# Kernel optimization log

Hardware: AMD Instinct MI355X
Metric: run time of the kernel (lower is better)

Reference implementation:

```python
import jax, jax.numpy as jnp
import numpy as np
from jax import lax

B, IMG, CIN, C, HEADS, K = 2, 112, 64, 256, 8, 3  # kernel_size[0]=3 used by hatt1
HD = C // HEADS


def layer_norm(x, w, b, eps=1e-5):
    mu = jnp.mean(x, axis=-1, keepdims=True)
    var = jnp.mean((x - mu) ** 2, axis=-1, keepdims=True)
    return (x - mu) / jnp.sqrt(var + eps) * w + b


def conv3x3(x, w, b):
    # x: (B,Cin,H,W), w: (Cout,Cin,3,3) -- stride 1, pad 1 (OverlapPatchEmbed patchsize=3)
    y = lax.conv_general_dilated(x, w, (1, 1), ((1, 1), (1, 1)),
                                 dimension_numbers=('NCHW', 'OIHW', 'NCHW'))
    return y + b[None, :, None, None]


def nat_cross_attention(q_in, kv_in, wq, bq, wkv, bkv, rpb, wp, bp, heads=HEADS, k=K):
    # NATTEN-style 2D neighborhood attention with separate query / key-value maps.
    Bb, H, W, Cc = q_in.shape
    hd = Cc // heads
    scale = hd ** -0.5
    q = (q_in @ wq + bq).reshape(Bb, H, W, heads, hd) * scale
    kv = (kv_in @ wkv + bkv).reshape(Bb, H, W, 2, heads, hd)
    kk, v = kv[:, :, :, 0], kv[:, :, :, 1]
    half = k // 2
    # border-clamped window starts -> every pixel attends to a full k x k window
    si = jnp.clip(jnp.arange(H) - half, 0, H - k)  # (H,)
    sj = jnp.clip(jnp.arange(W) - half, 0, W - k)  # (W,)
    nbi = si[:, None] + jnp.arange(k)  # (H,k) neighbor rows
    nbj = sj[:, None] + jnp.arange(k)  # (W,k) neighbor cols

    def gather(t):  # t: (B,H,W,heads,hd) -> (B,H,W,heads,k*k,hd)
        g = t[:, nbi]            # (B,H,k,W,heads,hd)
        g = g[:, :, :, nbj]      # (B,H,k,W,k,heads,hd)
        return jnp.transpose(g, (0, 1, 3, 5, 2, 4, 6)).reshape(Bb, H, W, heads, k * k, hd)

    kg, vg = gather(kk), gather(v)
    logits = jnp.einsum('bijhd,bijhnd->bijhn', q, kg)
    # relative position bias: rpb (heads, 2k-1, 2k-1)
    pi = jnp.arange(H) - si  # query position inside its window, 0..k-1
    pj = jnp.arange(W) - sj
    idx_i = jnp.arange(k)[None, :] - pi[:, None] + (k - 1)  # (H,k) in [0, 2k-2]
    idx_j = jnp.arange(k)[None, :] - pj[:, None] + (k - 1)  # (W,k)
    bias = rpb[:, idx_i]           # (heads,H,k,2k-1)
    bias = bias[:, :, :, idx_j]    # (heads,H,k,W,k)
    bias = jnp.transpose(bias, (1, 3, 0, 2, 4)).reshape(H, W, heads, k * k)
    attn = jax.nn.softmax(logits + bias, axis=-1)
    out = jnp.einsum('bijhn,bijhnd->bijhd', attn, vg).reshape(Bb, H, W, Cc)
    return out @ wp + bp


def setup_inputs() -> dict:
    key = jax.random.key(0)
    ks = jax.random.split(key, 24)
    std = 0.02
    inp = {
        'xq': jax.random.normal(ks[0], (B, CIN, IMG, IMG), jnp.float32),
        'xkv': jax.random.normal(ks[1], (B, CIN, IMG, IMG), jnp.float32),
        'conv1_w': jax.random.normal(ks[2], (C, CIN, 3, 3), jnp.float32) * std,
        'conv1_b': jnp.zeros((C,), jnp.float32),
        'conv3_w': jax.random.normal(ks[3], (C, CIN, 3, 3), jnp.float32) * std,
        'conv3_b': jnp.zeros((C,), jnp.float32),
        'ln1_w': jnp.ones((C,), jnp.float32), 'ln1_b': jnp.zeros((C,), jnp.float32),
        'ln10_w': jnp.ones((C,), jnp.float32), 'ln10_b': jnp.zeros((C,), jnp.float32),
        'ln3_w': jnp.ones((C,), jnp.float32), 'ln3_b': jnp.zeros((C,), jnp.float32),
        'wq': jax.random.normal(ks[4], (C, C), jnp.float32) * std,
        'bq': jnp.zeros((C,), jnp.float32),
        'wkv': jax.random.normal(ks[5], (C, 2 * C), jnp.float32) * std,
        'bkv': jnp.zeros((2 * C,), jnp.float32),
        'rpb': jax.random.normal(ks[6], (HEADS, 2 * K - 1, 2 * K - 1), jnp.float32) * std,
        'wp': jax.random.normal(ks[7], (C, C), jnp.float32) * std,
        'bp': jnp.zeros((C,), jnp.float32),
        'fc1_w': jax.random.normal(ks[8], (C, 2 * C), jnp.float32) * std,
        'fc1_b': jnp.zeros((2 * C,), jnp.float32),
        'fc2_w': jax.random.normal(ks[9], (2 * C, C), jnp.float32) * std,
        'fc2_b': jnp.zeros((C,), jnp.float32),
    }
    return inp


def reference(xq, xkv, conv1_w, conv1_b, conv3_w, conv3_b, ln1_w, ln1_b, ln10_w, ln10_b,
              ln3_w, ln3_b, wq, bq, wkv, bkv, rpb, wp, bp, fc1_w, fc1_b, fc2_w, fc2_b):
    # patch embeds (stride-1 3x3 conv, pad 1), channels-last maps (B,H,W,C)
    x1 = jnp.transpose(conv3x3(xq, conv1_w, conv1_b), (0, 2, 3, 1))
    x3 = jnp.transpose(conv3x3(xkv, conv3_w, conv3_b), (0, 2, 3, 1))
    qn = layer_norm(x1, ln1_w, ln1_b)    # norm1(x_embedding1)
    kvn = layer_norm(x1, ln10_w, ln10_b)  # norm1_0(x_embedding1)
    att1 = nat_cross_attention(qn, kvn, wq, bq, wkv, bkv, rpb, wp, bp)
    att = att1 + x3  # drop_path is identity at inference
    h = layer_norm(att, ln3_w, ln3_b)
    m = jax.nn.gelu(h @ fc1_w + fc1_b, approximate=False) @ fc2_w + fc2_b
    x = m + att
    return jnp.transpose(x, (0, 3, 1, 2))  # (B,C,H,W)
```

## Files before the change

kernel.cpp:

```cpp
#include <hip/hip_runtime.h>
#include <math.h>

#define IMG 112
#define CIN 64
#define CH 256
#define PADW 114
#define IMG2 12544
#define NPIX 25088
#define SCQ 0.17677669529663687f

typedef __bf16 bf16;
typedef __bf16 bf16x8 __attribute__((ext_vector_type(8)));
typedef float f32x4 __attribute__((ext_vector_type(4)));

__device__ __forceinline__ void gld_lds16(const void* g, void* l) {
    __builtin_amdgcn_global_load_lds(
        (const __attribute__((address_space(1))) void*)g,
        (__attribute__((address_space(3))) void*)l,
        16, 0, 0);
}
#define VMCNT0() asm volatile("s_waitcnt vmcnt(0)" ::: "memory")
#define BAR() __builtin_amdgcn_s_barrier()

__global__ __launch_bounds__(256) void prep_kernel(
    const float* __restrict__ xq, const float* __restrict__ xkv,
    bf16* __restrict__ padq, bf16* __restrict__ padkv,
    const float* __restrict__ c1w, const float* __restrict__ c3w,
    bf16* __restrict__ cw1, bf16* __restrict__ cw2,
    const float* __restrict__ wq, bf16* __restrict__ wqt,
    const float* __restrict__ wkv, bf16* __restrict__ wkvt,
    const float* __restrict__ wp, bf16* __restrict__ wpt,
    const float* __restrict__ f1w, bf16* __restrict__ wf1,
    const float* __restrict__ f2w, bf16* __restrict__ wf2) {
    int bid = blockIdx.x, tid = threadIdx.x;
    __shared__ float lds[CIN * 113];
    if (bid < 448) {
        const float* in = (bid < 224) ? xq : xkv;
        bf16* out = (bid < 224) ? padq : padkv;
        int bi = (bid < 224) ? bid : bid - 224;
        int b = bi / IMG, i = bi % IMG;
        const float* src = in + (size_t)b * CIN * IMG2 + (size_t)i * IMG;
        for (int t = tid; t < CIN * IMG; t += 256) {
            int ci = t / IMG, j = t - ci * IMG;
            lds[ci * 113 + j] = src[(size_t)ci * IMG2 + j];
        }
        __syncthreads();
        bf16* dst = out + (((size_t)(b * PADW + (i + 1)) * PADW) + 1) * CIN;
        for (int t = tid; t < CIN * IMG; t += 256) {
            int j = t / CIN, ci = t - j * CIN;
            dst[(size_t)j * CIN + ci] = (bf16)lds[ci * 113 + j];
        }
        bf16* rowbase = out + ((size_t)(b * PADW + (i + 1)) * PADW) * CIN;
        if (tid < 128) rowbase[(tid >> 6 ? 113 * CIN : 0) + (tid & 63)] = (bf16)0.0f;
        if (i == 0)
            for (int t = tid; t < PADW * CIN; t += 256)
                out[((size_t)(b * PADW + 0) * PADW) * CIN + t] = (bf16)0.0f;
        if (i == IMG - 1)
            for (int t = tid; t < PADW * CIN; t += 256)
                out[((size_t)(b * PADW + 113) * PADW) * CIN + t] = (bf16)0.0f;
    } else if (bid < 1024) {
        int idx = (bid - 448) * 256 + tid;
        int co = idx / 576, r = idx - co * 576;
        int tap = r >> 6, ci = r & 63;
        int src = co * 576 + ci * 9 + tap;
        cw1[idx] = (bf16)c1w[src];
        cw2[idx] = (bf16)c3w[src];
    } else {
        int off = (bid - 1024) * 256 + tid;
        const float* in; bf16* out; int K, N; float sc = 1.0f; int base;
        if (off < 65536)       { in = wq;  out = wqt;  K = 256; N = 256; sc = SCQ; base = 0; }
        else if (off < 196608) { in = wkv; out = wkvt; K = 256; N = 512; base = 65536; }
        else if (off < 262144) { in = wp;  out = wpt;  K = 256; N = 256; base = 196608; }
        else if (off < 393216) { in = f1w; out = wf1;  K = 256; N = 512; base = 262144; }
        else                   { in = f2w; out = wf2;  K = 512; N = 256; base = 393216; }
        int idx = off - base;
        int n = idx / K, k = idx - n * K;
        out[idx] = (bf16)(in[(size_t)k * N + n] * sc);
    }
}

#define M_DENSE 0
#define M_LN2   1
#define M_WPLN  2
#define M_GELU  3
#define M_NCHW  4

template <int AMODE, int MODE>
__device__ __forceinline__ void gemm_core(
    char* sm,
    const bf16* __restrict__ A, const bf16* __restrict__ B,
    const float* __restrict__ bias, float bscale,
    const bf16* __restrict__ res,
    bf16* __restrict__ out0, int ldo0,
    bf16* __restrict__ out1, float* __restrict__ outf,
    const float* __restrict__ lnw0, const float* __restrict__ lnb0,
    const float* __restrict__ lnw1, const float* __restrict__ lnb1,
    int K) {
    bf16* As = (bf16*)sm;
    bf16* Bs = (bf16*)(sm + 16384);
    float* lnb = (float*)sm;
    float* T = (float*)(sm + 2048);

    const int tid = threadIdx.x;
    const int wave = tid >> 6, lane = tid & 63;
    const int m0 = blockIdx.x * 64;
    const int wm = wave >> 1, wn = wave & 1;
    const int fr = lane & 15, fq = lane >> 4;
    const int srow = lane >> 3;
    const int scol = ((lane & 7) ^ srow) * 8;

    const bf16* aptr[2];
#pragma unroll
    for (int q = 0; q < 2; ++q) {
        int arow = m0 + wave * 16 + q * 8 + srow;
        if (AMODE == 1) {
            int b = arow / IMG2;
            int rem = arow - b * IMG2;
            int i = rem / IMG, j = rem - i * IMG;
            aptr[q] = A + ((size_t)((b * PADW + i) * PADW + j)) * CIN + scol;
        } else {
            aptr[q] = A + (size_t)arow * K + scol;
        }
    }
    const bf16* bptr0 = B + (size_t)(wave * 64 + srow) * K + scol;

    auto STAGE = [&](int bi, int kt) {
        int aoff = (AMODE == 1) ? ((kt / 3) * PADW + (kt - (kt / 3) * 3)) * CIN : kt * 64;
        int boff = kt * 64;
        bf16* ad = As + bi * 4096 + (wave * 16) * 64;
        gld_lds16(aptr[0] + aoff, ad);
        gld_lds16(aptr[1] + aoff, ad + 8 * 64);
        bf16* bd = Bs + bi * 16384 + (wave * 64) * 64;
#pragma unroll
        for (int u = 0; u < 8; ++u)
            gld_lds16(bptr0 + (size_t)u * 8 * K + boff, bd + u * 8 * 64);
    };

    f32x4 acc[2][8] = {};
    auto COMPUTE = [&](int bi) {
        const bf16* ab = As + bi * 4096;
        const bf16* bb = Bs + bi * 16384;
#pragma unroll
        for (int ks = 0; ks < 2; ++ks) {
            int ch = ((ks * 4 + fq) ^ (fr & 7)) * 8;
            bf16x8 af[2];
#pragma unroll
            for (int mi = 0; mi < 2; ++mi) af[mi] = *(const bf16x8*)&ab[(wm * 32 + mi * 16 + fr) * 64 + ch];
            bf16x8 bv[8];
#pragma unroll
            for (int ni = 0; ni < 8; ++ni) bv[ni] = *(const bf16x8*)&bb[(wn * 128 + ni * 16 + fr) * 64 + ch];
#pragma unroll
            for (int mi = 0; mi < 2; ++mi)
#pragma unroll
                for (int ni = 0; ni < 8; ++ni)
                    acc[mi][ni] = __builtin_amdgcn_mfma_f32_16x16x32_bf16(af[mi], bv[ni], acc[mi][ni], 0, 0, 0);
        }
    };

    const int nk = K >> 6;
    STAGE(0, 0);
    VMCNT0();
    BAR();
    int cur = 0;
    for (int kt = 0; kt < nk - 1; ++kt) {
        STAGE(cur ^ 1, kt + 1);
        COMPUTE(cur);
        VMCNT0();
        BAR();
        cur ^= 1;
    }
    COMPUTE(cur);

    float bvv[8];
#pragma unroll
    for (int ni = 0; ni < 8; ++ni) bvv[ni] = bias[wn * 128 + ni * 16 + fr] * bscale;
#pragma unroll
    for (int mi = 0; mi < 2; ++mi)
#pragma unroll
        for (int ni = 0; ni < 8; ++ni)
#pragma unroll
            for (int r = 0; r < 4; ++r) {
                float x = acc[mi][ni][r] + bvv[ni];
                if (MODE == M_WPLN) {
                    int prow = m0 + wm * 32 + mi * 16 + fq * 4 + r;
                    int col = wn * 128 + ni * 16 + fr;
                    x += (float)res[(size_t)prow * 256 + col];
                }
                if (MODE == M_GELU) x = 0.5f * x * (1.0f + erff(x * 0.70710678118f));
                acc[mi][ni][r] = x;
            }

    float mean_[2][4], rstd_[2][4];
    if (MODE == M_LN2 || MODE == M_WPLN) {
        BAR();
#pragma unroll
        for (int mi = 0; mi < 2; ++mi)
#pragma unroll
            for (int r = 0; r < 4; ++r) {
                float s = 0.0f, ss = 0.0f;
#pragma unroll
                for (int ni = 0; ni < 8; ++ni) {
                    float x = acc[mi][ni][r];
                    s += x; ss += x * x;
                }
#pragma unroll
                for (int msk = 1; msk <= 8; msk <<= 1) {
                    s += __shfl_xor(s, msk);
                    ss += __shfl_xor(ss, msk);
                }
                if (fr == 0) {
                    int row = wm * 32 + mi * 16 + fq * 4 + r;
                    lnb[wn * 128 + row] = s;
                    lnb[wn * 128 + 64 + row] = ss;
                }
            }
        BAR();
#pragma unroll
        for (int mi = 0; mi < 2; ++mi)
#pragma unroll
            for (int r = 0; r < 4; ++r) {
                int row = wm * 32 + mi * 16 + fq * 4 + r;
                float s = lnb[row] + lnb[128 + row];
                float ss = lnb[64 + row] + lnb[192 + row];
                float mean = s * (1.0f / CH);
                float var = ss * (1.0f / CH) - mean * mean;
                mean_[mi][r] = mean;
                rstd_[mi][r] = rsqrtf(var + 1e-5f);
            }
    } else {
        BAR();
    }

#pragma unroll
    for (int mi = 0; mi < 2; ++mi)
#pragma unroll
        for (int ni = 0; ni < 8; ++ni)
#pragma unroll
            for (int r = 0; r < 4; ++r) {
                int row = wm * 32 + mi * 16 + fq * 4 + r;
                int col = wn * 128 + ni * 16 + fr;
                float x = acc[mi][ni][r];
                if (MODE == M_LN2) x = (x - mean_[mi][r]) * rstd_[mi][r];
                T[row * 257 + col] = x;
            }
    BAR();

    if (MODE == M_NCHW) {
        int c = tid;
        int b = m0 / IMG2, p0 = m0 - b * IMG2;
        float* outp = outf + ((size_t)(b * CH + c)) * IMG2 + p0;
        const bf16* rp = res + (size_t)m0 * 256 + c;
#pragma unroll
        for (int g = 0; g < 16; ++g) {
            f32x4 v;
#pragma unroll
            for (int e = 0; e < 4; ++e)
                v[e] = T[(g * 4 + e) * 257 + c] + (float)rp[(size_t)(g * 4 + e) * 256];
            *(f32x4*)(outp + g * 4) = v;
        }
    } else {
        int row = tid & 63, qd = tid >> 6;
        int cb = qd * 64;
        if (MODE == M_DENSE || MODE == M_GELU) {
            bf16* op = out0 + (size_t)(m0 + row) * ldo0 + cb;
#pragma unroll
            for (int g = 0; g < 8; ++g) {
                bf16x8 o;
#pragma unroll
                for (int e = 0; e < 8; ++e) o[e] = (bf16)T[row * 257 + cb + g * 8 + e];
                *(bf16x8*)(op + g * 8) = o;
            }
        } else if (MODE == M_LN2) {
            bf16* op0 = out0 + (size_t)(m0 + row) * 256 + cb;
            bf16* op1 = out1 + (size_t)(m0 + row) * 256 + cb;
#pragma unroll
            for (int g = 0; g < 8; ++g) {
                bf16x8 o0, o1;
#pragma unroll
                for (int e = 0; e < 8; ++e) {
                    int c = cb + g * 8 + e;
                    float xh = T[row * 257 + c];
                    o0[e] = (bf16)(xh * lnw0[c] + lnb0[c]);
                    o1[e] = (bf16)(xh * lnw1[c] + lnb1[c]);
                }
                *(bf16x8*)(op0 + g * 8) = o0;
                *(bf16x8*)(op1 + g * 8) = o1;
            }
        } else if (MODE == M_WPLN) {
            float s = lnb[row] + lnb[128 + row];
            float ss = lnb[64 + row] + lnb[192 + row];
            float mean = s * (1.0f / CH);
            float rstd = rsqrtf(ss * (1.0f / CH) - mean * mean + 1e-5f);
            bf16* op0 = out0 + (size_t)(m0 + row) * 256 + cb;
            bf16* op1 = out1 + (size_t)(m0 + row) * 256 + cb;
#pragma unroll
            for (int g = 0; g < 8; ++g) {
                bf16x8 o0, o1;
#pragma unroll
                for (int e = 0; e < 8; ++e) {
                    int c = cb + g * 8 + e;
                    float x = T[row * 257 + c];
                    o0[e] = (bf16)x;
                    o1[e] = (bf16)((x - mean) * rstd * lnw0[c] + lnb0[c]);
                }
                *(bf16x8*)(op0 + g * 8) = o0;
                *(bf16x8*)(op1 + g * 8) = o1;
            }
        }
    }
}

__global__ __launch_bounds__(256) void conv_kernel(
    const bf16* padq, const bf16* padkv, const bf16* cw1, const bf16* cw2,
    const float* c1b, const float* c3b,
    bf16* qn, bf16* kvn, bf16* x3,
    const float* l1w, const float* l1b, const float* l10w, const float* l10b) {
    __shared__ char sm[81920];
    if (blockIdx.y == 0)
        gemm_core<1, M_LN2>(sm, padq, cw1, c1b, 1.0f, nullptr, qn, 256, kvn, nullptr,
                            l1w, l1b, l10w, l10b, 576);
    else
        gemm_core<1, M_DENSE>(sm, padkv, cw2, c3b, 1.0f, nullptr, x3, 256, nullptr, nullptr,
                              nullptr, nullptr, nullptr, nullptr, 576);
}

__global__ __launch_bounds__(256) void qkv_kernel(
    const bf16* qnp, const bf16* kvnp, const bf16* wqt, const bf16* wkvt,
    const float* bq, const float* bkv, bf16* q, bf16* kv) {
    __shared__ char sm[81920];
    int by = blockIdx.y;
    const bf16* A = by ? kvnp : qnp;
    const bf16* B = by ? (wkvt + (size_t)(by - 1) * 65536) : wqt;
    const float* bias = by ? (bkv + (by - 1) * 256) : bq;
    float bsc = by ? 1.0f : SCQ;
    bf16* out = by ? (kv + (by - 1) * 256) : q;
    int ldo = by ? 512 : 256;
    gemm_core<0, M_DENSE>(sm, A, B, bias, bsc, nullptr, out, ldo, nullptr, nullptr,
                          nullptr, nullptr, nullptr, nullptr, 256);
}

__global__ __launch_bounds__(256) void wp_kernel(
    const bf16* ao, const bf16* wpt, const float* bp, const bf16* x3,
    bf16* att, bf16* h, const float* l3w, const float* l3b) {
    __shared__ char sm[81920];
    gemm_core<0, M_WPLN>(sm, ao, wpt, bp, 1.0f, x3, att, 256, h, nullptr,
                         l3w, l3b, nullptr, nullptr, 256);
}

__global__ __launch_bounds__(256) void fc1_kernel(
    const bf16* h, const bf16* wf1, const float* f1b, bf16* m1) {
    __shared__ char sm[81920];
    int by = blockIdx.y;
    gemm_core<0, M_GELU>(sm, h, wf1 + (size_t)by * 65536, f1b + by * 256, 1.0f, nullptr,
                         m1 + by * 256, 512, nullptr, nullptr,
                         nullptr, nullptr, nullptr, nullptr, 256);
}

__global__ __launch_bounds__(256) void fc2_kernel(
    const bf16* m1, const bf16* wf2, const float* f2b, const bf16* att, float* out) {
    __shared__ char sm[81920];
    gemm_core<0, M_NCHW>(sm, m1, wf2, f2b, 1.0f, att, nullptr, 0, nullptr, out,
                         nullptr, nullptr, nullptr, nullptr, 512);
}

__global__ __launch_bounds__(256) void attn_kernel(const bf16* __restrict__ q, const bf16* __restrict__ kv,
                                                   const float* __restrict__ rpb, bf16* __restrict__ out) {
    int idx = blockIdx.x * 256 + threadIdx.x;
    int h = idx & 7, p = idx >> 3;
    int b = p / IMG2;
    int rem = p - b * IMG2;
    int i = rem / IMG, j = rem - i * IMG;
    int si = i - 1; if (si < 0) si = 0; if (si > IMG - 3) si = IMG - 3;
    int sj = j - 1; if (sj < 0) sj = 0; if (sj > IMG - 3) sj = IMG - 3;
    int pi = i - si, pj = j - sj;

    float qv[32];
    {
        const bf16x8* qp = (const bf16x8*)(q + (size_t)p * CH + h * 32);
#pragma unroll
        for (int g = 0; g < 4; ++g) {
            bf16x8 t = qp[g];
#pragma unroll
            for (int e = 0; e < 8; ++e) qv[g * 8 + e] = (float)t[e];
        }
    }
    float logits[9];
#pragma unroll
    for (int a = 0; a < 3; ++a) {
#pragma unroll
        for (int bb = 0; bb < 3; ++bb) {
            int pn = (b * IMG + (si + a)) * IMG + (sj + bb);
            const bf16x8* kp = (const bf16x8*)(kv + (size_t)pn * 512 + h * 32);
            float s = 0.0f;
#pragma unroll
            for (int g = 0; g < 4; ++g) {
                bf16x8 t = kp[g];
#pragma unroll
                for (int e = 0; e < 8; ++e) s += qv[g * 8 + e] * (float)t[e];
            }
            logits[a * 3 + bb] = s + rpb[(h * 5 + (a - pi + 2)) * 5 + (bb - pj + 2)];
        }
    }
    float mx = logits[0];
#pragma unroll
    for (int n = 1; n < 9; ++n) mx = fmaxf(mx, logits[n]);
    float den = 0.0f;
#pragma unroll
    for (int n = 0; n < 9; ++n) { logits[n] = expf(logits[n] - mx); den += logits[n]; }
    float inv = 1.0f / den;
    float o[32] = {};
#pragma unroll
    for (int a = 0; a < 3; ++a) {
#pragma unroll
        for (int bb = 0; bb < 3; ++bb) {
            int pn = (b * IMG + (si + a)) * IMG + (sj + bb);
            float wgt = logits[a * 3 + bb] * inv;
            const bf16x8* vp = (const bf16x8*)(kv + (size_t)pn * 512 + 256 + h * 32);
#pragma unroll
            for (int g = 0; g < 4; ++g) {
                bf16x8 t = vp[g];
#pragma unroll
                for (int e = 0; e < 8; ++e) o[g * 8 + e] += wgt * (float)t[e];
            }
        }
    }
    bf16* op = out + (size_t)p * CH + h * 32;
#pragma unroll
    for (int g = 0; g < 4; ++g) {
        bf16x8 t;
#pragma unroll
        for (int e = 0; e < 8; ++e) t[e] = (bf16)o[g * 8 + e];
        *(bf16x8*)(op + g * 8) = t;
    }
}

extern "C" void kernel_launch(void* const* d_in, const int* in_sizes, int n_in,
                              void* d_out, int out_size, void* d_ws, size_t ws_size,
                              hipStream_t stream) {
    (void)in_sizes; (void)n_in; (void)out_size; (void)ws_size;
    const float* xq    = (const float*)d_in[0];
    const float* xkv   = (const float*)d_in[1];
    const float* c1w   = (const float*)d_in[2];
    const float* c1b   = (const float*)d_in[3];
    const float* c3w   = (const float*)d_in[4];
    const float* c3b   = (const float*)d_in[5];
    const float* ln1w  = (const float*)d_in[6];
    const float* ln1b  = (const float*)d_in[7];
    const float* ln10w = (const float*)d_in[8];
    const float* ln10b = (const float*)d_in[9];
    const float* ln3w  = (const float*)d_in[10];
    const float* ln3b  = (const float*)d_in[11];
    const float* wq    = (const float*)d_in[12];
    const float* bq    = (const float*)d_in[13];
    const float* wkv   = (const float*)d_in[14];
    const float* bkv   = (const float*)d_in[15];
    const float* rpb   = (const float*)d_in[16];
    const float* wp    = (const float*)d_in[17];
    const float* bp    = (const float*)d_in[18];
    const float* f1w   = (const float*)d_in[19];
    const float* f1b   = (const float*)d_in[20];
    const float* f2w   = (const float*)d_in[21];
    const float* f2b   = (const float*)d_in[22];
    float* out = (float*)d_out;

    char* ws = (char*)d_ws;
    bf16* PADQ  = (bf16*)(ws + 0);
    bf16* PADKV = (bf16*)(ws + 3326976);
    bf16* CW1   = (bf16*)(ws + 6653952);
    bf16* CW2   = (bf16*)(ws + 6948864);
    bf16* WQT   = (bf16*)(ws + 7243776);
    bf16* WKVT  = (bf16*)(ws + 7374848);
    bf16* WPT   = (bf16*)(ws + 7636992);
    bf16* WF1   = (bf16*)(ws + 7768064);
    bf16* WF2   = (bf16*)(ws + 8030208);
    bf16* QN    = (bf16*)(ws + 8292352);
    bf16* KVN   = (bf16*)(ws + 21137408);
    bf16* Q     = (bf16*)(ws + 33982464);
    bf16* KV    = (bf16*)(ws + 46827520);
    bf16* AO    = (bf16*)(ws + 72517632);
    bf16* X3    = (bf16*)(ws + 85362688);
    bf16* ATT   = (bf16*)(ws + 98207744);
    bf16* H     = (bf16*)(ws + 111052800);
    bf16* M1    = (bf16*)(ws + 123897856);

    prep_kernel<<<3072, 256, 0, stream>>>(xq, xkv, PADQ, PADKV, c1w, c3w, CW1, CW2,
                                          wq, WQT, wkv, WKVT, wp, WPT, f1w, WF1, f2w, WF2);
    conv_kernel<<<dim3(392, 2), 256, 0, stream>>>(PADQ, PADKV, CW1, CW2, c1b, c3b,
                                                  QN, KVN, X3, ln1w, ln1b, ln10w, ln10b);
    qkv_kernel<<<dim3(392, 3), 256, 0, stream>>>(QN, KVN, WQT, WKVT, bq, bkv, Q, KV);
    attn_kernel<<<784, 256, 0, stream>>>(Q, KV, rpb, AO);
    wp_kernel<<<392, 256, 0, stream>>>(AO, WPT, bp, X3, ATT, H, ln3w, ln3b);
    fc1_kernel<<<dim3(392, 2), 256, 0, stream>>>(H, WF1, f1b, M1);
    fc2_kernel<<<392, 256, 0, stream>>>(M1, WF2, f2b, ATT, out);
}
```

Baseline: 291.1 us.

## Shrink GEMM shared memory to single buffer and bf16 epilogue tile for occupancy

Drops the double-buffered K-tile pipeline in favour of a single LDS buffer with stage/wait/compute/barrier per step. The epilogue transpose tile is stored as XOR-swizzled bf16 instead of padded fp32, and the NCHW epilogue is done in two halves. Together these cut shared memory from 80KB to 40KB so three blocks can share a CU, which launch bounds now request. The cost is that global loads no longer overlap MFMA compute within a block, so latency hiding depends on the extra resident blocks. Rounding the LN2 intermediate to bf16 before the affine step also adds a little error.

Result: slower. 305.2 us (+4.8%).

```diff
diff --git a/kernel.cpp b/kernel.cpp
--- a/kernel.cpp
+++ b/kernel.cpp
@@ -84,6 +84,8 @@
 #define M_WPLN  2
 #define M_GELU  3
 #define M_NCHW  4
+#define TS 264
+#define TFS 258
 
 template <int AMODE, int MODE>
 __device__ __forceinline__ void gemm_core(
@@ -97,9 +99,10 @@
     const float* __restrict__ lnw1, const float* __restrict__ lnb1,
     int K) {
     bf16* As = (bf16*)sm;
-    bf16* Bs = (bf16*)(sm + 16384);
+    bf16* Bs = (bf16*)(sm + 8192);
     float* lnb = (float*)sm;
-    float* T = (float*)(sm + 2048);
+    bf16* Tb = (bf16*)(sm + 2048);
+    float* Tf = (float*)(sm + 2048);
 
     const int tid = threadIdx.x;
     const int wave = tid >> 6, lane = tid & 63;
@@ -124,31 +127,29 @@
     }
     const bf16* bptr0 = B + (size_t)(wave * 64 + srow) * K + scol;
 
-    auto STAGE = [&](int bi, int kt) {
+    auto STAGE = [&](int kt) {
         int aoff = (AMODE == 1) ? ((kt / 3) * PADW + (kt - (kt / 3) * 3)) * CIN : kt * 64;
         int boff = kt * 64;
-        bf16* ad = As + bi * 4096 + (wave * 16) * 64;
+        bf16* ad = As + (wave * 16) * 64;
         gld_lds16(aptr[0] + aoff, ad);
         gld_lds16(aptr[1] + aoff, ad + 8 * 64);
-        bf16* bd = Bs + bi * 16384 + (wave * 64) * 64;
+        bf16* bd = Bs + (wave * 64) * 64;
 #pragma unroll
         for (int u = 0; u < 8; ++u)
             gld_lds16(bptr0 + (size_t)u * 8 * K + boff, bd + u * 8 * 64);
     };
 
     f32x4 acc[2][8] = {};
-    auto COMPUTE = [&](int bi) {
-        const bf16* ab = As + bi * 4096;
-        const bf16* bb = Bs + bi * 16384;
+    auto COMPUTE = [&]() {
 #pragma unroll
         for (int ks = 0; ks < 2; ++ks) {
             int ch = ((ks * 4 + fq) ^ (fr & 7)) * 8;
             bf16x8 af[2];
 #pragma unroll
-            for (int mi = 0; mi < 2; ++mi) af[mi] = *(const bf16x8*)&ab[(wm * 32 + mi * 16 + fr) * 64 + ch];
+            for (int mi = 0; mi < 2; ++mi) af[mi] = *(const bf16x8*)&As[(wm * 32 + mi * 16 + fr) * 64 + ch];
             bf16x8 bv[8];
 #pragma unroll
-            for (int ni = 0; ni < 8; ++ni) bv[ni] = *(const bf16x8*)&bb[(wn * 128 + ni * 16 + fr) * 64 + ch];
+            for (int ni = 0; ni < 8; ++ni) bv[ni] = *(const bf16x8*)&Bs[(wn * 128 + ni * 16 + fr) * 64 + ch];
 #pragma unroll
             for (int mi = 0; mi < 2; ++mi)
 #pragma unroll
@@ -158,18 +159,13 @@
     };
 
     const int nk = K >> 6;
-    STAGE(0, 0);
-    VMCNT0();
-    BAR();
-    int cur = 0;
-    for (int kt = 0; kt < nk - 1; ++kt) {
-        STAGE(cur ^ 1, kt + 1);
-        COMPUTE(cur);
+    for (int kt = 0; kt < nk; ++kt) {
+        STAGE(kt);
         VMCNT0();
         BAR();
-        cur ^= 1;
-    }
-    COMPUTE(cur);
+        COMPUTE();
+        BAR();
+    }
 
     float bvv[8];
 #pragma unroll
@@ -192,7 +188,6 @@
 
     float mean_[2][4], rstd_[2][4];
     if (MODE == M_LN2 || MODE == M_WPLN) {
-        BAR();
 #pragma unroll
         for (int mi = 0; mi < 2; ++mi)
 #pragma unroll
@@ -227,23 +222,7 @@
                 mean_[mi][r] = mean;
                 rstd_[mi][r] = rsqrtf(var + 1e-5f);
             }
-    } else {
-        BAR();
-    }
-
-#pragma unroll
-    for (int mi = 0; mi < 2; ++mi)
-#pragma unroll
-        for (int ni = 0; ni < 8; ++ni)
-#pragma unroll
-            for (int r = 0; r < 4; ++r) {
-                int row = wm * 32 + mi * 16 + fq * 4 + r;
-                int col = wn * 128 + ni * 16 + fr;
-                float x = acc[mi][ni][r];
-                if (MODE == M_LN2) x = (x - mean_[mi][r]) * rstd_[mi][r];
-                T[row * 257 + col] = x;
-            }
-    BAR();
+    }
 
     if (MODE == M_NCHW) {
         int c = tid;
@@ -251,37 +230,62 @@
         float* outp = outf + ((size_t)(b * CH + c)) * IMG2 + p0;
         const bf16* rp = res + (size_t)m0 * 256 + c;
 #pragma unroll
-        for (int g = 0; g < 16; ++g) {
-            f32x4 v;
-#pragma unroll
-            for (int e = 0; e < 4; ++e)
-                v[e] = T[(g * 4 + e) * 257 + c] + (float)rp[(size_t)(g * 4 + e) * 256];
-            *(f32x4*)(outp + g * 4) = v;
+        for (int p = 0; p < 2; ++p) {
+            if (wm == p) {
+#pragma unroll
+                for (int mi = 0; mi < 2; ++mi)
+#pragma unroll
+                    for (int ni = 0; ni < 8; ++ni)
+#pragma unroll
+                        for (int r = 0; r < 4; ++r)
+                            Tf[(mi * 16 + fq * 4 + r) * TFS + wn * 128 + ni * 16 + fr] = acc[mi][ni][r];
+            }
+            BAR();
+#pragma unroll
+            for (int g = 0; g < 8; ++g) {
+                f32x4 v;
+#pragma unroll
+                for (int e = 0; e < 4; ++e)
+                    v[e] = Tf[(g * 4 + e) * TFS + c] + (float)rp[(size_t)(p * 32 + g * 4 + e) * 256];
+                *(f32x4*)(outp + p * 32 + g * 4) = v;
+            }
+            BAR();
         }
     } else {
+#pragma unroll
+        for (int mi = 0; mi < 2; ++mi)
+#pragma unroll
+            for (int ni = 0; ni < 8; ++ni)
+#pragma unroll
+                for (int r = 0; r < 4; ++r) {
+                    int row = wm * 32 + mi * 16 + fq * 4 + r;
+                    int col = wn * 128 + ni * 16 + fr;
+                    float x = acc[mi][ni][r];
+                    if (MODE == M_LN2) x = (x - mean_[mi][r]) * rstd_[mi][r];
+                    Tb[row * TS + (col ^ ((row & 7) << 3))] = (bf16)x;
+                }
+        BAR();
         int row = tid & 63, qd = tid >> 6;
         int cb = qd * 64;
+        int xr = (row & 7) << 3;
         if (MODE == M_DENSE || MODE == M_GELU) {
             bf16* op = out0 + (size_t)(m0 + row) * ldo0 + cb;
 #pragma unroll
-            for (int g = 0; g < 8; ++g) {
-                bf16x8 o;
-#pragma unroll
-                for (int e = 0; e < 8; ++e) o[e] = (bf16)T[row * 257 + cb + g * 8 + e];
-                *(bf16x8*)(op + g * 8) = o;
-            }
+            for (int g = 0; g < 8; ++g)
+                *(bf16x8*)(op + g * 8) = *(const bf16x8*)&Tb[row * TS + ((cb + g * 8) ^ xr)];
         } else if (MODE == M_LN2) {
             bf16* op0 = out0 + (size_t)(m0 + row) * 256 + cb;
             bf16* op1 = out1 + (size_t)(m0 + row) * 256 + cb;
 #pragma unroll
             for (int g = 0; g < 8; ++g) {
+                bf16x8 xh = *(const bf16x8*)&Tb[row * TS + ((cb + g * 8) ^ xr)];
                 bf16x8 o0, o1;
 #pragma unroll
                 for (int e = 0; e < 8; ++e) {
                     int c = cb + g * 8 + e;
-                    float xh = T[row * 257 + c];
-                    o0[e] = (bf16)(xh * lnw0[c] + lnb0[c]);
-                    o1[e] = (bf16)(xh * lnw1[c] + lnb1[c]);
+                    float v = (float)xh[e];
+                    o0[e] = (bf16)(v * lnw0[c] + lnb0[c]);
+                    o1[e] = (bf16)(v * lnw1[c] + lnb1[c]);
                 }
                 *(bf16x8*)(op0 + g * 8) = o0;
                 *(bf16x8*)(op1 + g * 8) = o1;
@@ -295,27 +299,28 @@
             bf16* op1 = out1 + (size_t)(m0 + row) * 256 + cb;
 #pragma unroll
             for (int g = 0; g < 8; ++g) {
-                bf16x8 o0, o1;
+                bf16x8 xv = *(const bf16x8*)&Tb[row * TS + ((cb + g * 8) ^ xr)];
+                bf16x8 o1;
 #pragma unroll
                 for (int e = 0; e < 8; ++e) {
                     int c = cb + g * 8 + e;
-                    float x = T[row * 257 + c];
-                    o0[e] = (bf16)x;
-                    o1[e] = (bf16)((x - mean) * rstd * lnw0[c] + lnb0[c]);
-                }
-                *(bf16x8*)(op0 + g * 8) = o0;
+                    o1[e] = (bf16)(((float)xv[e] - mean) * rstd * lnw0[c] + lnb0[c]);
+                }
+                *(bf16x8*)(op0 + g * 8) = xv;
                 *(bf16x8*)(op1 + g * 8) = o1;
             }
         }
     }
 }
 
-__global__ __launch_bounds__(256) void conv_kernel(
+#define SMEMSZ 40960
+
+__global__ __launch_bounds__(256, 3) void conv_kernel(
     const bf16* padq, const bf16* padkv, const bf16* cw1, const bf16* cw2,
     const float* c1b, const float* c3b,
     bf16* qn, bf16* kvn, bf16* x3,
     const float* l1w, const float* l1b, const float* l10w, const float* l10b) {
-    __shared__ char sm[81920];
+    __shared__ __align__(16) char sm[SMEMSZ];
     if (blockIdx.y == 0)
         gemm_core<1, M_LN2>(sm, padq, cw1, c1b, 1.0f, nullptr, qn, 256, kvn, nullptr,
                             l1w, l1b, l10w, l10b, 576);
@@ -324,10 +329,10 @@
                               nullptr, nullptr, nullptr, nullptr, 576);
 }
 
-__global__ __launch_bounds__(256) void qkv_kernel(
+__global__ __launch_bounds__(256, 3) void qkv_kernel(
     const bf16* qnp, const bf16* kvnp, const bf16* wqt, const bf16* wkvt,
     const float* bq, const float* bkv, bf16* q, bf16* kv) {
-    __shared__ char sm[81920];
+    __shared__ __align__(16) char sm[SMEMSZ];
     int by = blockIdx.y;
     const bf16* A = by ? kvnp : qnp;
     const bf16* B = by ? (wkvt + (size_t)(by - 1) * 65536) : wqt;
@@ -339,26 +344,26 @@
                           nullptr, nullptr, nullptr, nullptr, 256);
 }
 
-__global__ __launch_bounds__(256) void wp_kernel(
+__global__ __launch_bounds__(256, 3) void wp_kernel(
     const bf16* ao, const bf16* wpt, const float* bp, const bf16* x3,
     bf16* att, bf16* h, const float* l3w, const float* l3b) {
-    __shared__ char sm[81920];
+    __shared__ __align__(16) char sm[SMEMSZ];
     gemm_core<0, M_WPLN>(sm, ao, wpt, bp, 1.0f, x3, att, 256, h, nullptr,
                          l3w, l3b, nullptr, nullptr, 256);
 }
 
-__global__ __launch_bounds__(256) void fc1_kernel(
+__global__ __launch_bounds__(256, 3) void fc1_kernel(
     const bf16* h, const bf16* wf1, const float* f1b, bf16* m1) {
-    __shared__ char sm[81920];
+    __shared__ __align__(16) char sm[SMEMSZ];
     int by = blockIdx.y;
     gemm_core<0, M_GELU>(sm, h, wf1 + (size_t)by * 65536, f1b + by * 256, 1.0f, nullptr,
                          m1 + by * 256, 512, nullptr, nullptr,
                          nullptr, nullptr, nullptr, nullptr, 256);
 }
 
-__global__ __launch_bounds__(256) void fc2_kernel(
+__global__ __launch_bounds__(256, 3) void fc2_kernel(
     const bf16* m1, const bf16* wf2, const float* f2b, const bf16* att, float* out) {
-    __shared__ char sm[81920];
+    __shared__ __align__(16) char sm[SMEMSZ];
     gemm_core<0, M_NCHW>(sm, m1, wf2, f2b, 1.0f, att, nullptr, 0, nullptr, out,
                          nullptr, nullptr, nullptr, nullptr, 512);
 }
```
